# Kernel tuning notes

Measured on AMD Instinct MI355X. Metric: run time of the kernel, lower is better.

## Reference

```python
import jax, jax.numpy as jnp
import numpy as np

B, S, E, H, M = 4, 2048, 1024, 16, 32  # batch, seq, hidden, heads, max_rel_dist
D = E // H  # head dim


def setup_inputs() -> dict:
    key = jax.random.key(0)
    ks = jax.random.split(key, 4)
    x = jax.random.normal(ks[0], (B, S, E), dtype=jnp.float32)
    in_proj_w = jax.random.normal(ks[1], (3 * E, E), dtype=jnp.float32) * (E ** -0.5)
    in_proj_b = jnp.zeros((3 * E,), dtype=jnp.float32)
    out_w = jax.random.normal(ks[2], (E, E), dtype=jnp.float32) * (E ** -0.5)
    out_b = jnp.zeros((E,), dtype=jnp.float32)
    rel_bias = jax.random.normal(ks[3], (2 * M + 1, H), dtype=jnp.float32) * 0.02
    return {"x": x, "in_proj_w": in_proj_w, "in_proj_b": in_proj_b,
            "out_w": out_w, "out_b": out_b, "rel_bias": rel_bias}


def reference(x, in_proj_w, in_proj_b, out_w, out_b, rel_bias):
    b, s, e = x.shape
    # relative position index: clamp(i-j, -M, M) + M  -> [S, S]
    rel_pos = jnp.clip(jnp.arange(s)[:, None] - jnp.arange(s)[None, :], -M, M) + M
    # gather per-head bias then average over heads (matches the per-head sum / H loop)
    attn_mask = rel_bias[rel_pos].mean(axis=-1)  # [S, S]

    # fused QKV projection (torch in_proj: x @ W^T + b)
    qkv = x @ in_proj_w.T + in_proj_b  # [B, S, 3E]
    q, k, v = jnp.split(qkv, 3, axis=-1)
    # reshape to heads: [B, H, S, D]
    q = q.reshape(b, s, H, D).transpose(0, 2, 1, 3)
    k = k.reshape(b, s, H, D).transpose(0, 2, 1, 3)
    v = v.reshape(b, s, H, D).transpose(0, 2, 1, 3)

    scores = jnp.einsum("bhqd,bhkd->bhqk", q, k) * (D ** -0.5) + attn_mask
    attn = jax.nn.softmax(scores, axis=-1)
    out = jnp.einsum("bhqk,bhkd->bhqd", attn, v)  # [B, H, S, D]
    out = out.transpose(0, 2, 1, 3).reshape(b, s, e)
    return out @ out_w.T + out_b
```

## Files before the change

kernel.cpp:

```cpp
#include <hip/hip_runtime.h>
#include <hip/hip_fp16.h>
#include <stdint.h>
#include <stddef.h>


typedef _Float16 half8 __attribute__((ext_vector_type(8)));
typedef _Float16 half2v __attribute__((ext_vector_type(2)));
typedef float f32x4 __attribute__((ext_vector_type(4)));
typedef float f32x16 __attribute__((ext_vector_type(16)));
typedef uint32_t u32x4 __attribute__((ext_vector_type(4)));

#define MFMA16(a, b, c) __builtin_amdgcn_mfma_f32_16x16x32_f16(a, b, c, 0, 0, 0)
#define MFMA32(a, b, c) __builtin_amdgcn_mfma_f32_32x32x16_f16(a, b, c, 0, 0, 0)

__device__ static inline void gload_lds16(const void* g, void* l) {
  __builtin_amdgcn_global_load_lds(
      (const __attribute__((address_space(1))) void*)g,
      (__attribute__((address_space(3))) void*)l, 16, 0, 0);
}

__device__ static inline uint32_t pkrtz(float a, float b) {
  return __builtin_bit_cast(uint32_t, __builtin_amdgcn_cvt_pkrtz(a, b));
}

__global__ void cvt_all(const float* __restrict__ x, const float* __restrict__ w,
                        const float* __restrict__ ow, const float* __restrict__ rb,
                        __half* __restrict__ xh, __half* __restrict__ wh,
                        __half* __restrict__ owh, float* __restrict__ mbg,
                        int nx, int nw, int no) {
  if (blockIdx.x == 0 && threadIdx.x < 65) {
    float s = 0.f;
    #pragma unroll
    for (int hh = 0; hh < 16; ++hh) s += rb[threadIdx.x * 16 + hh];
    mbg[threadIdx.x] = s * (1.44269504f / 16.f);
  }
  const int total = nx + nw + no;
  int i = blockIdx.x * blockDim.x + threadIdx.x;
  const int stride = gridDim.x * blockDim.x;
  for (; i < total; i += stride) {
    const float* src; __half* dst; int j;
    if (i < nx)            { src = x;  dst = xh;  j = i; }
    else if (i < nx + nw)  { src = w;  dst = wh;  j = i - nx; }
    else                   { src = ow; dst = owh; j = i - nx - nw; }
    const float4* p = (const float4*)src + (size_t)j * 2;
    float4 a = p[0], b = p[1];
    half8 hv;
    hv[0] = (_Float16)a.x; hv[1] = (_Float16)a.y; hv[2] = (_Float16)a.z; hv[3] = (_Float16)a.w;
    hv[4] = (_Float16)b.x; hv[5] = (_Float16)b.y; hv[6] = (_Float16)b.z; hv[7] = (_Float16)b.w;
    *(half8*)(dst + (size_t)j * 8) = hv;
  }
}

template <bool OUT_HALF>
__global__ __launch_bounds__(256)
void gemm_bt(const __half* __restrict__ A, const __half* __restrict__ Bm,
             const float* __restrict__ bias, void* __restrict__ Cout,
             int Ndim, int K) {
  __shared__ __align__(16) __half As[128 * 32];
  __shared__ __align__(16) __half Bs[128 * 32];
  const int tid = threadIdx.x;
  const int lane = tid & 63;
  const int wave = tid >> 6;
  const int wr = wave >> 1, wc = wave & 1;
  const int flat = blockIdx.y * gridDim.x + blockIdx.x;
  const int cpx = (gridDim.x * gridDim.y) >> 3;
  const int nid = (flat & 7) * cpx + (flat >> 3);
  const int bn = nid % gridDim.x;
  const int bm = nid / gridDim.x;
  const int l15 = lane & 15;
  const int kseg = lane >> 4;

  f32x4 acc[4][4];
  #pragma unroll
  for (int i = 0; i < 4; ++i)
    #pragma unroll
    for (int j = 0; j < 4; ++j) {
      acc[i][j][0] = 0.f; acc[i][j][1] = 0.f; acc[i][j][2] = 0.f; acc[i][j][3] = 0.f;
    }

  const int nk = K >> 5;
  for (int kt = 0; kt < nk; ++kt) {
    __syncthreads();
    #pragma unroll
    for (int c = 0; c < 2; ++c) {
      const int off = c * 4096 + tid * 16;
      const int mloc = off >> 6;
      const int kb = off & 63;
      gload_lds16(A + (size_t)(bm * 128 + mloc) * K + kt * 32 + (kb >> 1),
                  (char*)As + c * 4096 + wave * 1024);
      gload_lds16(Bm + (size_t)(bn * 128 + mloc) * K + kt * 32 + (kb >> 1),
                  (char*)Bs + c * 4096 + wave * 1024);
    }
    __syncthreads();
    half8 af[4], bf[4];
    #pragma unroll
    for (int i = 0; i < 4; ++i) {
      af[i] = *(const half8*)&As[(wr * 64 + i * 16 + l15) * 32 + kseg * 8];
      bf[i] = *(const half8*)&Bs[(wc * 64 + i * 16 + l15) * 32 + kseg * 8];
    }
    #pragma unroll
    for (int i = 0; i < 4; ++i)
      #pragma unroll
      for (int j = 0; j < 4; ++j)
        acc[i][j] = MFMA16(af[i], bf[j], acc[i][j]);
  }

  const int crow0 = bm * 128 + wr * 64;
  const int ccol0 = bn * 128 + wc * 64;
  #pragma unroll
  for (int j = 0; j < 4; ++j) {
    const int c = ccol0 + j * 16 + l15;
    const float bv = bias[c];
    #pragma unroll
    for (int i = 0; i < 4; ++i) {
      #pragma unroll
      for (int r = 0; r < 4; ++r) {
        const int row = crow0 + i * 16 + kseg * 4 + r;
        const float v = acc[i][j][r] + bv;
        if (OUT_HALF)
          ((__half*)Cout)[(size_t)row * Ndim + c] = __float2half_rn(v);
        else
          ((float*)Cout)[(size_t)row * Ndim + c] = v;
      }
    }
  }
}

#define CHUNK(sv, c) do {                                                   \
    const int base2_ = qw - kb - 16 * (c);                                  \
    float ex_[8];                                                           \
    if (base2_ >= 47) {                                                     \
      _Pragma("unroll")                                                     \
      for (int j_ = 0; j_ < 8; ++j_)                                        \
        ex_[j_] = __builtin_amdgcn_exp2f(                                   \
            fmaf(sv[8 * ((c) & 1) + j_], kscale, mbs_hi));                  \
    } else if (base2_ <= -63) {                                             \
      _Pragma("unroll")                                                     \
      for (int j_ = 0; j_ < 8; ++j_)                                        \
        ex_[j_] = __builtin_amdgcn_exp2f(                                   \
            fmaf(sv[8 * ((c) & 1) + j_], kscale, mbs_lo));                  \
    } else {                                                                \
      _Pragma("unroll")                                                     \
      for (int j_ = 0; j_ < 8; ++j_) {                                      \
        int d_ = qs - (kb + 16 * (c) + 8 * (j_ >> 2) + (j_ & 3) + 4 * hi);  \
        d_ = min(max(d_, -32), 32);                                         \
        ex_[j_] = __builtin_amdgcn_exp2f(                                   \
            fmaf(sv[8 * ((c) & 1) + j_], kscale, mb[d_ + 32]));             \
      }                                                                     \
    }                                                                       \
    _Pragma("unroll")                                                       \
    for (int j_ = 0; j_ < 8; ++j_) lp4[j_ & 3] += ex_[j_];                  \
    uint32_t QA0_ = pkrtz(ex_[0], ex_[1]);                                  \
    uint32_t QA1_ = pkrtz(ex_[2], ex_[3]);                                  \
    uint32_t QB0_ = pkrtz(ex_[4], ex_[5]);                                  \
    uint32_t QB1_ = pkrtz(ex_[6], ex_[7]);                                  \
    auto r0_ = __builtin_amdgcn_permlane32_swap(QA0_, QB0_, false, false);  \
    auto r1_ = __builtin_amdgcn_permlane32_swap(QA1_, QB1_, false, false);  \
    u32x4 uv_;                                                              \
    uv_[0] = r0_[0]; uv_[1] = r1_[0]; uv_[2] = r0_[1]; uv_[3] = r1_[1];     \
    half8 ap_ = __builtin_bit_cast(half8, uv_);                             \
    const int cby_ = (32 * (c) + 16 * hi) ^ swzv;                           \
    half8 bv0_ = *(const half8*)(vtb + l31 * 128 + cby_);                   \
    half8 bv1_ = *(const half8*)(vtb + (32 + l31) * 128 + cby_);            \
    o0 = MFMA32(ap_, bv0_, o0);                                             \
    o1 = MFMA32(ap_, bv1_, o1);                                             \
  } while (0)

__global__ __launch_bounds__(512)
void attn_kernel(const __half* __restrict__ qkv, const float* __restrict__ mb,
                 __half* __restrict__ attn_out) {
  __shared__ __align__(16) __half Ks[4][64 * 64];
  __shared__ __align__(16) __half Vts[4][64 * 64];

  const int tid = threadIdx.x;
  const int lane = tid & 63;
  const int w = tid >> 6;
  const int l31 = lane & 31;
  const int hi = lane >> 5;
  const int flat = (blockIdx.y << 3) | blockIdx.x;
  const int nid = (flat & 7) * 64 + (flat >> 3);
  const int bh = nid >> 3;
  const int b = bh >> 4, h = bh & 15;
  const int qw = (nid & 7) * 256 + w * 32;
  const int qs = qw + l31;
  const float kscale = 0.125f * 1.44269504f;
  const int swzv = (l31 & 7) << 4;

  const float mbs_lo = mb[0];
  const float mbs_hi = mb[64];

  const size_t qrow = (size_t)(b * 2048 + qs) * 3072;
  half8 bq[4];
  #pragma unroll
  for (int s = 0; s < 4; ++s)
    bq[s] = *(const half8*)&qkv[qrow + h * 64 + s * 16 + hi * 8];

  const int krow0 = tid >> 3;
  const int kcolsw = ((tid & 7) * 16) ^ ((krow0 & 7) << 4);
  const __half* kp0 = qkv + (size_t)(b * 2048 + krow0) * 3072 + 1024 + h * 64 + (kcolsw >> 1);

  const int vds = w * 8;
  const __half* vp = qkv + (size_t)(b * 2048 + lane) * 3072 + 2048 + h * 64 + vds;

  const size_t kvstep = (size_t)64 * 3072;

  f32x4 lp4 = {0.f, 0.f, 0.f, 0.f};
  f32x16 o0, o1;
  #pragma unroll
  for (int i = 0; i < 16; ++i) { o0[i] = 0.f; o1[i] = 0.f; }

  gload_lds16(kp0, (char*)Ks[0] + w * 1024);
  gload_lds16(kp0 + kvstep, (char*)Ks[1] + w * 1024);
  half8 va = *(const half8*)vp;
  half8 vb = *(const half8*)(vp + kvstep);
  #pragma unroll
  for (int e = 0; e < 8; ++e) {
    *(__half*)((char*)Vts[0] + (vds + e) * 128 + ((lane * 2) ^ (e << 4))) = (__half)va[e];
    *(__half*)((char*)Vts[1] + (vds + e) * 128 + ((lane * 2) ^ (e << 4))) = (__half)vb[e];
  }
  va = *(const half8*)(vp + 2 * kvstep);
  vb = *(const half8*)(vp + 3 * kvstep);

  auto compute_tile = [&](int kb, const char* ksb, const char* vtb) {
    f32x16 s0, s1;
    #pragma unroll
    for (int i = 0; i < 16; ++i) { s0[i] = 0.f; s1[i] = 0.f; }
    __builtin_amdgcn_s_setprio(1);
    #pragma unroll
    for (int s = 0; s < 4; ++s) {
      const int cby = (s * 32 + hi * 16) ^ swzv;
      half8 ak0 = *(const half8*)(ksb + l31 * 128 + cby);
      half8 ak1 = *(const half8*)(ksb + (32 + l31) * 128 + cby);
      s0 = MFMA32(ak0, bq[s], s0);
      s1 = MFMA32(ak1, bq[s], s1);
    }
    __builtin_amdgcn_s_setprio(0);
    __builtin_amdgcn_s_setprio(1);
    CHUNK(s0, 0);
    CHUNK(s0, 1);
    CHUNK(s1, 2);
    CHUNK(s1, 3);
    __builtin_amdgcn_s_setprio(0);
  };

  for (int kt = 0; kt < 32; kt += 2) {
    __syncthreads();

    if (kt < 30) {
      const size_t adv2 = (size_t)(kt + 2) * kvstep;
      const size_t adv3 = (size_t)(kt + 3) * kvstep;
      gload_lds16(kp0 + adv2, (char*)Ks[(kt + 2) & 3] + w * 1024);
      gload_lds16(kp0 + adv3, (char*)Ks[(kt + 3) & 3] + w * 1024);
      char* v2 = (char*)Vts[(kt + 2) & 3];
      char* v3 = (char*)Vts[(kt + 3) & 3];
      #pragma unroll
      for (int e = 0; e < 8; ++e) {
        const int sw = (lane * 2) ^ (e << 4);
        *(__half*)(v2 + (vds + e) * 128 + sw) = (__half)va[e];
        *(__half*)(v3 + (vds + e) * 128 + sw) = (__half)vb[e];
      }
      if (kt < 28) {
        va = *(const half8*)(vp + (size_t)(kt + 4) * kvstep);
        vb = *(const half8*)(vp + (size_t)(kt + 5) * kvstep);
      }
    }

    compute_tile(kt * 64, (const char*)Ks[kt & 3], (const char*)Vts[kt & 3]);
    compute_tile((kt + 1) * 64, (const char*)Ks[(kt + 1) & 3],
                 (const char*)Vts[(kt + 1) & 3]);
  }

  float lp = (lp4[0] + lp4[1]) + (lp4[2] + lp4[3]);
  lp += __shfl_xor(lp, 32, 64);
  float* lsh = ((float*)Ks[1]) + w * 32;
  if (hi == 0) lsh[l31] = lp;
  #pragma unroll
  for (int r = 0; r < 16; ++r) {
    const int ql = (r & 3) + 8 * (r >> 2) + 4 * hi;
    const float rl = 1.f / lsh[ql];
    const size_t row = (size_t)(b * 2048 + qw + ql) * 1024 + h * 64;
    attn_out[row + l31]      = __float2half(o0[r] * rl);
    attn_out[row + 32 + l31] = __float2half(o1[r] * rl);
  }
}

extern "C" void kernel_launch(void* const* d_in, const int* in_sizes, int n_in,
                              void* d_out, int out_size, void* d_ws, size_t ws_size,
                              hipStream_t stream) {
  const float* x    = (const float*)d_in[0];
  const float* in_w = (const float*)d_in[1];
  const float* in_b = (const float*)d_in[2];
  const float* ow   = (const float*)d_in[3];
  const float* ob   = (const float*)d_in[4];
  const float* rb   = (const float*)d_in[5];

  char* ws = (char*)d_ws;
  __half* xh   = (__half*)(ws);
  __half* wh   = (__half*)(ws + 16777216);
  __half* owh  = (__half*)(ws + 23068672);
  float*  mb   = (float*)(ws + 25165824);
  __half* qkvh = (__half*)(ws + 25166336);
  __half* atth = (__half*)(ws + 75497984);

  cvt_all<<<2048, 256, 0, stream>>>(x, in_w, ow, rb, xh, wh, owh, mb,
                                    (8192 * 1024) / 8, (3072 * 1024) / 8,
                                    (1024 * 1024) / 8);

  gemm_bt<true><<<dim3(24, 64), 256, 0, stream>>>(xh, wh, in_b, qkvh, 3072, 1024);
  attn_kernel<<<dim3(8, 64), 512, 0, stream>>>(qkvh, mb, atth);
  gemm_bt<false><<<dim3(8, 64), 256, 0, stream>>>(atth, owh, ob, (float*)d_out, 1024, 1024);
}
```

Measured before the change: 218.4 us.

## Triple-buffer LDS tiles in GEMM with two-stage-ahead async prefetch

The projection GEMM now keeps three LDS buffers for the A and B tiles and issues the async global-to-LDS loads for tile kt+2 while computing on tile kt. This replaces the old load, sync, compute pattern and drops one barrier per K step, so memory latency can overlap with MFMA work. Per-thread source addresses are hoisted out of the loop. In exchange LDS use per block triples, which can lower occupancy, and the overlap depth depends on how the barrier waits on outstanding LDS-DMA loads.

Result: faster. 208.2 us (median of 3 runs) (-4.7%).

```diff
diff --git a/kernel.cpp b/kernel.cpp
--- a/kernel.cpp
+++ b/kernel.cpp
@@ -56,8 +56,8 @@
 void gemm_bt(const __half* __restrict__ A, const __half* __restrict__ Bm,
              const float* __restrict__ bias, void* __restrict__ Cout,
              int Ndim, int K) {
-  __shared__ __align__(16) __half As[128 * 32];
-  __shared__ __align__(16) __half Bs[128 * 32];
+  __shared__ __align__(16) __half As[3][128 * 32];
+  __shared__ __align__(16) __half Bs[3][128 * 32];
   const int tid = threadIdx.x;
   const int lane = tid & 63;
   const int wave = tid >> 6;
@@ -70,6 +70,24 @@
   const int l15 = lane & 15;
   const int kseg = lane >> 4;
 
+  const int off0 = tid * 16;
+  const int mloc0 = off0 >> 6, kb0 = off0 & 63;
+  const int off1 = 4096 + tid * 16;
+  const int mloc1 = off1 >> 6, kb1 = off1 & 63;
+  const __half* a0 = A + (size_t)(bm * 128 + mloc0) * K + (kb0 >> 1);
+  const __half* a1 = A + (size_t)(bm * 128 + mloc1) * K + (kb1 >> 1);
+  const __half* b0 = Bm + (size_t)(bn * 128 + mloc0) * K + (kb0 >> 1);
+  const __half* b1 = Bm + (size_t)(bn * 128 + mloc1) * K + (kb1 >> 1);
+
+  auto stage = [&](int kt, int buf) {
+    char* ad = (char*)As[buf] + wave * 1024;
+    char* bd = (char*)Bs[buf] + wave * 1024;
+    gload_lds16(a0 + kt * 32, ad);
+    gload_lds16(a1 + kt * 32, ad + 4096);
+    gload_lds16(b0 + kt * 32, bd);
+    gload_lds16(b1 + kt * 32, bd + 4096);
+  };
+
   f32x4 acc[4][4];
   #pragma unroll
   for (int i = 0; i < 4; ++i)
@@ -79,30 +97,30 @@
     }
 
   const int nk = K >> 5;
+  stage(0, 0);
+  stage(1, 1);
+
+  int buf = 0;
   for (int kt = 0; kt < nk; ++kt) {
     __syncthreads();
-    #pragma unroll
-    for (int c = 0; c < 2; ++c) {
-      const int off = c * 4096 + tid * 16;
-      const int mloc = off >> 6;
-      const int kb = off & 63;
-      gload_lds16(A + (size_t)(bm * 128 + mloc) * K + kt * 32 + (kb >> 1),
-                  (char*)As + c * 4096 + wave * 1024);
-      gload_lds16(Bm + (size_t)(bn * 128 + mloc) * K + kt * 32 + (kb >> 1),
-                  (char*)Bs + c * 4096 + wave * 1024);
-    }
-    __syncthreads();
+    if (kt + 2 < nk) {
+      int nb = buf + 2; if (nb >= 3) nb -= 3;
+      stage(kt + 2, nb);
+    }
+    const __half* as = As[buf];
+    const __half* bs = Bs[buf];
     half8 af[4], bf[4];
     #pragma unroll
     for (int i = 0; i < 4; ++i) {
-      af[i] = *(const half8*)&As[(wr * 64 + i * 16 + l15) * 32 + kseg * 8];
-      bf[i] = *(const half8*)&Bs[(wc * 64 + i * 16 + l15) * 32 + kseg * 8];
+      af[i] = *(const half8*)&as[(wr * 64 + i * 16 + l15) * 32 + kseg * 8];
+      bf[i] = *(const half8*)&bs[(wc * 64 + i * 16 + l15) * 32 + kseg * 8];
     }
     #pragma unroll
     for (int i = 0; i < 4; ++i)
       #pragma unroll
       for (int j = 0; j < 4; ++j)
         acc[i][j] = MFMA16(af[i], bf[j], acc[i][j]);
+    if (++buf == 3) buf = 0;
   }
 
   const int crow0 = bm * 128 + wr * 64;
```
